# Performance work log

Hardware: AMD Instinct MI355X
Metric: run time of the kernel (lower is better)

## Reference

```python
import jax, jax.numpy as jnp
import numpy as np

EMB = 1024
HEAD = 64

def setup_inputs() -> dict:
    key = jax.random.key(0)
    ks = jax.random.split(key, 7)
    s = 1.0 / np.sqrt(EMB)
    X = jax.random.normal(ks[0], (4, 4096, EMB), dtype=jnp.float32)
    Wk = jax.random.uniform(ks[1], (EMB, HEAD), jnp.float32, -s, s)
    bk = jax.random.uniform(ks[2], (HEAD,), jnp.float32, -s, s)
    Wq = jax.random.uniform(ks[3], (EMB, HEAD), jnp.float32, -s, s)
    bq = jax.random.uniform(ks[4], (HEAD,), jnp.float32, -s, s)
    Wv = jax.random.uniform(ks[5], (EMB, HEAD), jnp.float32, -s, s)
    bv = jax.random.uniform(ks[6], (HEAD,), jnp.float32, -s, s)
    return {"X": X, "Wk": Wk, "bk": bk, "Wq": Wq, "bq": bq, "Wv": Wv, "bv": bv}

def reference(X, Wk, bk, Wq, bq, Wv, bv):
    # X: [B, S, E]; projections -> [B, S, H]
    k = X @ Wk + bk
    q = X @ Wq + bq
    v = X @ Wv + bv
    S = X.shape[1]
    scale = 1.0 / np.sqrt(HEAD).astype(np.float32)
    scores = jnp.einsum('bqh,bkh->bqk', q, k) * scale  # [B, S, S]
    causal = jnp.tril(jnp.ones((S, S), dtype=bool))
    scores = jnp.where(causal, scores, -jnp.inf)
    probs = jax.nn.softmax(scores, axis=-1)
    return jnp.einsum('bqk,bkh->bqh', probs, v)
```

## Files before the change

### kernel.cpp

```cpp
#include <hip/hip_runtime.h>

#define S_LEN 4096
#define EMBD  1024
#define HEADD 64

typedef __bf16 bf16x8 __attribute__((ext_vector_type(8)));
typedef float  f32x4  __attribute__((ext_vector_type(4)));

__device__ __forceinline__ unsigned short f2bf(float f) {
  union { float f; unsigned u; } x; x.f = f;
  unsigned r = x.u + 0x7FFFu + ((x.u >> 16) & 1u);
  return (unsigned short)(r >> 16);
}

__device__ __forceinline__ bf16x8 cvt8(f32x4 a, f32x4 b) {
  union { bf16x8 v; unsigned short s[8]; } u;
#pragma unroll
  for (int j = 0; j < 4; j++) { u.s[j] = f2bf(a[j]); u.s[4 + j] = f2bf(b[j]); }
  return u.v;
}

__device__ __forceinline__ unsigned fbits(float f) {
  union { float f; unsigned u; } x; x.f = f; return x.u;
}

__global__ void prep_w(const float* __restrict__ Wk, const float* __restrict__ bk,
                       const float* __restrict__ Wq, const float* __restrict__ bq,
                       const float* __restrict__ Wv, const float* __restrict__ bv,
                       unsigned short* __restrict__ wt, float* __restrict__ bias) {
  int n = blockIdx.x;
  int t = threadIdx.x;
  const float QSCALE = 0.125f * 1.44269504088896340736f;
  const float* W; const float* bsrc; int col; float s = 1.0f;
  if (n < 64)       { W = Wk; bsrc = bk; col = n; }
  else if (n < 128) { W = Wq; bsrc = bq; col = n - 64; s = QSCALE; }
  else              { W = Wv; bsrc = bv; col = n - 128; }
  for (int k = t; k < EMBD; k += 256)
    wt[n * EMBD + k] = f2bf(W[k * HEADD + col] * s);
  if (t == 0) bias[n] = bsrc[col] * s;
}

__global__ __launch_bounds__(256, 1) void proj_qkv(
    const float* __restrict__ X, const unsigned short* __restrict__ wt,
    const float* __restrict__ bias,
    unsigned short* __restrict__ qws, unsigned short* __restrict__ kws,
    unsigned short* __restrict__ vtws) {
  __shared__ unsigned short xs[64 * 512];

  const int tid = threadIdx.x;
  const int w = tid >> 6;
  const int lane = tid & 63;
  const int l15 = lane & 15, lg = lane >> 4;
  const int row0 = blockIdx.x * 64;

  const int sr = tid >> 5;
  const int sc = (tid & 31) * 8;

  const unsigned short* wp = wt + (size_t)(w * 48 + l15) * EMBD + lg * 8;

  f32x4 acc[4][3];
#pragma unroll
  for (int g = 0; g < 4; g++)
#pragma unroll
    for (int j = 0; j < 3; j++) acc[g][j] = (f32x4){0.f, 0.f, 0.f, 0.f};

  f32x4 la[16], lb[16];
#pragma unroll
  for (int it = 0; it < 16; it++) {
    const int r = (it & 7) * 8 + sr;
    const int c = (it >> 3) * 256 + sc;
    const float* src = X + (size_t)(row0 + r) * EMBD + c;
    la[it] = *(const f32x4*)src;
    lb[it] = *(const f32x4*)(src + 4);
  }
#pragma unroll
  for (int it = 0; it < 16; it++) {
    const int r = (it & 7) * 8 + sr;
    const int c = (it >> 3) * 256 + sc;
    int soff = (r << 9) + c;
    soff ^= (r & 7) << 3;
    *(bf16x8*)&xs[soff] = cvt8(la[it], lb[it]);
  }
  __syncthreads();

#pragma unroll
  for (int kc = 0; kc < 2; kc++) {
    if (kc + 1 < 2) {
#pragma unroll
      for (int it = 0; it < 16; it++) {
        const int r = (it & 7) * 8 + sr;
        const int c = 512 + (it >> 3) * 256 + sc;
        const float* src = X + (size_t)(row0 + r) * EMBD + c;
        la[it] = *(const f32x4*)src;
        lb[it] = *(const f32x4*)(src + 4);
      }
    }
    bf16x8 wf[2][3];
#pragma unroll
    for (int j = 0; j < 3; j++)
      wf[0][j] = *(const bf16x8*)(wp + (size_t)j * 16 * EMBD + kc * 512);
#pragma unroll
    for (int ss = 0; ss < 16; ss++) {
      const int cur = ss & 1;
      if (ss + 1 < 16) {
#pragma unroll
        for (int j = 0; j < 3; j++)
          wf[cur ^ 1][j] = *(const bf16x8*)(wp + (size_t)j * 16 * EMBD + kc * 512 + (ss + 1) * 32);
      }
      const int c = ss * 32 + lg * 8;
      bf16x8 a[4];
#pragma unroll
      for (int g = 0; g < 4; g++) {
        int so = ((g * 16 + l15) << 9) + c;
        so ^= (l15 & 7) << 3;
        a[g] = *(const bf16x8*)&xs[so];
      }
#pragma unroll
      for (int j = 0; j < 3; j++)
#pragma unroll
        for (int g = 0; g < 4; g++)
          acc[g][j] = __builtin_amdgcn_mfma_f32_16x16x32_bf16(a[g], wf[cur][j], acc[g][j], 0, 0, 0);
    }
    __syncthreads();
    if (kc + 1 < 2) {
#pragma unroll
      for (int it = 0; it < 16; it++) {
        const int r = (it & 7) * 8 + sr;
        const int c = (it >> 3) * 256 + sc;
        int soff = (r << 9) + c;
        soff ^= (r & 7) << 3;
        *(bf16x8*)&xs[soff] = cvt8(la[it], lb[it]);
      }
      __syncthreads();
    }
  }

#pragma unroll
  for (int g = 0; g < 4; g++) {
    const int crow0 = row0 + g * 16 + lg * 4;
#pragma unroll
    for (int j = 0; j < 3; j++) {
      const int nf = w * 3 + j;
      const int n = nf * 16 + l15;
      const float bs = bias[n];
      if (nf < 8) {
        unsigned short* dst = (nf < 4) ? kws : qws;
        const int nn = n & 63;
#pragma unroll
        for (int i = 0; i < 4; i++)
          dst[(size_t)(crow0 + i) * HEADD + nn] = f2bf(acc[g][j][i] + bs);
      } else {
        const int d = n - 128;
        const int bb = crow0 >> 12, sr2 = crow0 & 4095;
        union { unsigned long long pk; unsigned short s[4]; } u;
#pragma unroll
        for (int i = 0; i < 4; i++) u.s[i] = f2bf(acc[g][j][i] + bs);
        *(unsigned long long*)&vtws[((size_t)bb * HEADD + d) * S_LEN + sr2] = u.pk;
      }
    }
  }
}

__global__ __launch_bounds__(512, 1) void attn(
    const unsigned short* __restrict__ qws,
    const unsigned short* __restrict__ kws,
    const unsigned short* __restrict__ vtws,
    unsigned short* __restrict__ pO,
    float* __restrict__ pmv, float* __restrict__ plv) {
  __shared__ uint4 kvb[2][1024];
  __shared__ unsigned short pbl[8][16][72];

  const int tid = threadIdx.x;
  const int w = tid >> 6;
  const int lane = tid & 63;
  const int l15 = lane & 15, lg = lane >> 4;
  const int srow = tid >> 3;
  const int scol = (tid & 7) * 8;
  const int soff = ((srow * 128 + (tid & 7) * 16)) ^ ((srow & 7) << 4);

  const int id = blockIdx.x;
  const int b = id & 3;
  const int x = (id >> 2) & 15;
  const int h = id >> 6;

  const unsigned short* kb = kws + (size_t)b * S_LEN * HEADD;
  const unsigned short* vb = vtws + (size_t)b * HEADD * S_LEN;
  const unsigned short* qp = qws + (size_t)b * S_LEN * HEADD;

  const int PH = 31 - x, PL = x;
  const int tlPH = 2 * PH + 1;
  const int tlwH = 2 * PH + (w >> 2);
  const int tlwL = 2 * PL + (w >> 2);
  const int qbH = PH * 128 + w * 16;
  const int qbL = PL * 128 + w * 16;

  const unsigned short* qH = qp + (size_t)(qbH + l15) * HEADD + lg * 8;
  const unsigned short* qL = qp + (size_t)(qbL + l15) * HEADD + lg * 8;
  const bf16x8 bqH0 = *(const bf16x8*)qH, bqH1 = *(const bf16x8*)(qH + 32);
  const bf16x8 bqL0 = *(const bf16x8*)qL, bqL1 = *(const bf16x8*)(qL + 32);

  f32x4 oH[4], oL[4];
#pragma unroll
  for (int nd = 0; nd < 4; nd++) {
    oH[nd] = (f32x4){0.f, 0.f, 0.f, 0.f};
    oL[nd] = (f32x4){0.f, 0.f, 0.f, 0.f};
  }
  float mH = -3.0e38f, lH = 0.f, mL = -3.0e38f, lL = 0.f;

#define PROC(BQ0, BQ1, O, M, LL, QB, TLX, tt, base)                             \
  do {                                                                          \
    bf16x8 k0[4], k1[4], v0[4], v1[4];                                          \
    _Pragma("unroll")                                                           \
    for (int nf = 0; nf < 4; nf++) {                                            \
      const int r = nf * 16 + l15;                                              \
      const int sw = (l15 & 7) << 4;                                            \
      const int b0 = (r * 128 + lg * 16) ^ sw;                                  \
      const int b1 = (r * 128 + 64 + lg * 16) ^ sw;                             \
      k0[nf] = *(const bf16x8*)&base[b0];                                       \
      k1[nf] = *(const bf16x8*)&base[b1];                                       \
      v0[nf] = *(const bf16x8*)&base[8192 + b0];                                \
      v1[nf] = *(const bf16x8*)&base[8192 + b1];                                \
    }                                                                           \
    f32x4 sc[4];                                                                \
    __builtin_amdgcn_s_setprio(1);                                              \
    _Pragma("unroll")                                                           \
    for (int nf = 0; nf < 4; nf++) {                                            \
      f32x4 z = (f32x4){0.f, 0.f, 0.f, 0.f};                                    \
      z = __builtin_amdgcn_mfma_f32_16x16x32_bf16(k0[nf], BQ0, z, 0, 0, 0);     \
      sc[nf] = __builtin_amdgcn_mfma_f32_16x16x32_bf16(k1[nf], BQ1, z, 0, 0, 0);\
    }                                                                           \
    __builtin_amdgcn_s_setprio(0);                                              \
    if ((tt) == (TLX)) {                                                        \
      const int qa = (QB) + l15;                                                \
      _Pragma("unroll")                                                         \
      for (int nf = 0; nf < 4; nf++)                                            \
        _Pragma("unroll")                                                       \
        for (int i = 0; i < 4; i++)                                             \
          if ((tt) * 64 + nf * 16 + lg * 4 + i > qa) sc[nf][i] = -1.0e30f;      \
    }                                                                           \
    float pm = sc[0][0];                                                        \
    _Pragma("unroll")                                                           \
    for (int nf = 0; nf < 4; nf++)                                              \
      _Pragma("unroll")                                                         \
      for (int i = 0; i < 4; i++) pm = fmaxf(pm, sc[nf][i]);                    \
    if (!__all(pm <= M + 8.0f)) {                                               \
      float mx = fmaxf(pm, __shfl_xor(pm, 16));                                 \
      mx = fmaxf(mx, __shfl_xor(mx, 32));                                       \
      const float mn = fmaxf(M, mx);                                            \
      const float al = __builtin_amdgcn_exp2f(M - mn);                          \
      M = mn;                                                                   \
      LL *= al;                                                                 \
      float alr[4];                                                             \
      _Pragma("unroll")                                                         \
      for (int i = 0; i < 4; i++) alr[i] = __shfl(al, lg * 4 + i);              \
      _Pragma("unroll")                                                         \
      for (int nd = 0; nd < 4; nd++)                                            \
        _Pragma("unroll")                                                       \
        for (int i = 0; i < 4; i++) O[nd][i] *= alr[i];                         \
    }                                                                           \
    _Pragma("unroll")                                                           \
    for (int nf = 0; nf < 4; nf++) {                                            \
      f32x4 p;                                                                  \
      _Pragma("unroll")                                                         \
      for (int i = 0; i < 4; i++) p[i] = __builtin_amdgcn_exp2f(sc[nf][i] - M); \
      LL += p[0] + p[1] + p[2] + p[3];                                          \
      unsigned lo_ = __builtin_amdgcn_perm(fbits(p[1]) + 0x8000u,               \
                                           fbits(p[0]) + 0x8000u, 0x07060302u); \
      unsigned hi_ = __builtin_amdgcn_perm(fbits(p[3]) + 0x8000u,               \
                                           fbits(p[2]) + 0x8000u, 0x07060302u); \
      uint2 pk_; pk_.x = lo_; pk_.y = hi_;                                      \
      *(uint2*)&pbl[w][l15][nf * 16 + lg * 4] = pk_;                            \
    }                                                                           \
    const bf16x8 ap0 = *(const bf16x8*)&pbl[w][l15][lg * 8];                    \
    const bf16x8 ap1 = *(const bf16x8*)&pbl[w][l15][32 + lg * 8];               \
    __builtin_amdgcn_s_setprio(1);                                              \
    _Pragma("unroll")                                                           \
    for (int nd = 0; nd < 4; nd++) {                                            \
      f32x4 oo = __builtin_amdgcn_mfma_f32_16x16x32_bf16(ap0, v0[nd], O[nd], 0, 0, 0); \
      O[nd] = __builtin_amdgcn_mfma_f32_16x16x32_bf16(ap1, v1[nd], oo, 0, 0, 0);\
    }                                                                           \
    __builtin_amdgcn_s_setprio(0);                                              \
  } while (0)

#define LOADG(tt)                                                               \
  do {                                                                          \
    kreg = *(const uint4*)(kb + ((size_t)(tt) * 64 + srow) * HEADD + scol);     \
    vreg = *(const uint4*)(vb + (size_t)srow * S_LEN + (tt) * 64 + scol);       \
  } while (0)

#define WRITEL(bf)                                                              \
  do {                                                                          \
    unsigned char* d_ = (unsigned char*)kvb[bf];                                \
    *(uint4*)&d_[soff] = kreg;                                                  \
    *(uint4*)&d_[8192 + soff] = vreg;                                           \
  } while (0)

  {
    uint4 kreg, vreg;
    int t = h;
    LOADG(t);
    WRITEL(0);
    __syncthreads();
    int cur = 0;
#pragma unroll 1
    while (true) {
      const int tn = t + 4;
      const bool hn = tn <= tlPH;
      if (hn) LOADG(tn);
      {
        const unsigned char* base = (const unsigned char*)kvb[cur];
        if (t <= tlwH) PROC(bqH0, bqH1, oH, mH, lH, qbH, tlwH, t, base);
        if (t <= tlwL) PROC(bqL0, bqL1, oL, mL, lL, qbL, tlwL, t, base);
      }
      if (!hn) break;
      WRITEL(cur ^ 1);
      __syncthreads();
      cur ^= 1;
      t = tn;
    }
  }

  lH += __shfl_xor(lH, 16);
  lH += __shfl_xor(lH, 32);
  lL += __shfl_xor(lL, 16);
  lL += __shfl_xor(lL, 32);
  const size_t pbH = (size_t)(h * 4 + b) * S_LEN + qbH;
  const size_t pbL = (size_t)(h * 4 + b) * S_LEN + qbL;
  if (lane < 16) {
    pmv[pbH + lane] = mH; plv[pbH + lane] = lH;
    pmv[pbL + lane] = mL; plv[pbL + lane] = lL;
  }
#pragma unroll
  for (int nd = 0; nd < 4; nd++)
#pragma unroll
    for (int i = 0; i < 4; i++) {
      pO[(pbH + lg * 4 + i) * 64 + nd * 16 + l15] = f2bf(oH[nd][i]);
      pO[(pbL + lg * 4 + i) * 64 + nd * 16 + l15] = f2bf(oL[nd][i]);
    }
#undef PROC
#undef LOADG
#undef WRITEL
}

__global__ __launch_bounds__(256) void merge_attn(
    const unsigned short* __restrict__ pO,
    const float* __restrict__ pmv, const float* __restrict__ plv,
    float* __restrict__ out) {
  const int row = blockIdx.x * 64 + (threadIdx.x >> 2);
  const int q = threadIdx.x & 3;
  float mh[4], lh[4];
  float M = -3.0e38f;
#pragma unroll
  for (int hh = 0; hh < 4; hh++) {
    mh[hh] = pmv[hh * 16384 + row];
    lh[hh] = plv[hh * 16384 + row];
    M = fmaxf(M, mh[hh]);
  }
  float Lt = 0.f, a[4];
#pragma unroll
  for (int hh = 0; hh < 4; hh++) {
    a[hh] = __builtin_amdgcn_exp2f(mh[hh] - M);
    Lt += a[hh] * lh[hh];
  }
  const float iL = 1.0f / Lt;
  float acc[16];
#pragma unroll
  for (int c = 0; c < 16; c++) acc[c] = 0.f;
#pragma unroll
  for (int hh = 0; hh < 4; hh++) {
    const unsigned short* src = pO + ((size_t)hh * 16384 + row) * 64 + q * 16;
    const uint4 u0 = *(const uint4*)(src);
    const uint4 u1 = *(const uint4*)(src + 8);
    const unsigned* uu0 = (const unsigned*)&u0;
    const unsigned* uu1 = (const unsigned*)&u1;
#pragma unroll
    for (int j = 0; j < 4; j++) {
      union { unsigned u; float f; } e0, e1, e2, e3;
      e0.u = uu0[j] << 16;  e1.u = uu0[j] & 0xffff0000u;
      e2.u = uu1[j] << 16;  e3.u = uu1[j] & 0xffff0000u;
      acc[j * 2 + 0] += e0.f * a[hh];
      acc[j * 2 + 1] += e1.f * a[hh];
      acc[8 + j * 2 + 0] += e2.f * a[hh];
      acc[8 + j * 2 + 1] += e3.f * a[hh];
    }
  }
  float* dst = out + (size_t)row * 64 + q * 16;
#pragma unroll
  for (int c = 0; c < 16; c++) dst[c] = acc[c] * iL;
}

extern "C" void kernel_launch(void* const* d_in, const int* in_sizes, int n_in,
                              void* d_out, int out_size, void* d_ws, size_t ws_size,
                              hipStream_t stream) {
  const float* X  = (const float*)d_in[0];
  const float* Wk = (const float*)d_in[1];
  const float* bk = (const float*)d_in[2];
  const float* Wq = (const float*)d_in[3];
  const float* bq = (const float*)d_in[4];
  const float* Wv = (const float*)d_in[5];
  const float* bv = (const float*)d_in[6];
  float* out = (float*)d_out;

  char* ws = (char*)d_ws;
  unsigned short* kws  = (unsigned short*)(ws);
  unsigned short* qws  = (unsigned short*)(ws + (2u << 20));
  unsigned short* vtws = (unsigned short*)(ws + (4u << 20));
  unsigned short* wt   = (unsigned short*)(ws + (6u << 20));
  float*          bias = (float*)(ws + (6u << 20) + (512u << 10));
  unsigned short* pO   = (unsigned short*)(ws + (8u << 20));
  float*          pmv  = (float*)(ws + (16u << 20));
  float*          plv  = (float*)(ws + (17u << 20));

  prep_w<<<dim3(192), dim3(256), 0, stream>>>(Wk, bk, Wq, bq, Wv, bv, wt, bias);
  proj_qkv<<<dim3(256), dim3(256), 0, stream>>>(X, wt, bias, qws, kws, vtws);
  attn<<<dim3(256), dim3(512), 0, stream>>>(qws, kws, vtws, pO, pmv, plv);
  merge_attn<<<dim3(256), dim3(256), 0, stream>>>(pO, pmv, plv, out);
}
```

Measured before the change: 61.11 us.

## Split attention work into 64-row query tiles with one tile per warp

The attention kernel now launches 512 blocks instead of 256. Each warp handles a single 16-row query slice, taken from either the high or the low 64-row tile of a paired causal range, rather than processing both a high and a low slice. This halves per-warp register state (one accumulator set), and launch bounds now allow two blocks per CU to raise occupancy. The cost is that each block's shared K/V tile is reused by fewer query rows, and warps in the low half sit idle once their causal range ends.

```diff
diff --git a/kernel.cpp b/kernel.cpp
--- a/kernel.cpp
+++ b/kernel.cpp
@@ -161,7 +161,7 @@
   }
 }
 
-__global__ __launch_bounds__(512, 1) void attn(
+__global__ __launch_bounds__(512, 2) void attn(
     const unsigned short* __restrict__ qws,
     const unsigned short* __restrict__ kws,
     const unsigned short* __restrict__ vtws,
@@ -180,34 +180,29 @@
 
   const int id = blockIdx.x;
   const int b = id & 3;
-  const int x = (id >> 2) & 15;
-  const int h = id >> 6;
+  const int x = (id >> 2) & 31;
+  const int h = id >> 7;
 
   const unsigned short* kb = kws + (size_t)b * S_LEN * HEADD;
   const unsigned short* vb = vtws + (size_t)b * HEADD * S_LEN;
   const unsigned short* qp = qws + (size_t)b * S_LEN * HEADD;
 
-  const int PH = 31 - x, PL = x;
-  const int tlPH = 2 * PH + 1;
-  const int tlwH = 2 * PH + (w >> 2);
-  const int tlwL = 2 * PL + (w >> 2);
-  const int qbH = PH * 128 + w * 16;
-  const int qbL = PL * 128 + w * 16;
-
-  const unsigned short* qH = qp + (size_t)(qbH + l15) * HEADD + lg * 8;
-  const unsigned short* qL = qp + (size_t)(qbL + l15) * HEADD + lg * 8;
-  const bf16x8 bqH0 = *(const bf16x8*)qH, bqH1 = *(const bf16x8*)(qH + 32);
-  const bf16x8 bqL0 = *(const bf16x8*)qL, bqL1 = *(const bf16x8*)(qL + 32);
-
-  f32x4 oH[4], oL[4];
-#pragma unroll
-  for (int nd = 0; nd < 4; nd++) {
-    oH[nd] = (f32x4){0.f, 0.f, 0.f, 0.f};
-    oL[nd] = (f32x4){0.f, 0.f, 0.f, 0.f};
-  }
-  float mH = -3.0e38f, lH = 0.f, mL = -3.0e38f, lL = 0.f;
-
-#define PROC(BQ0, BQ1, O, M, LL, QB, TLX, tt, base)                             \
+  const int isL = w >> 2;
+  const int P = isL ? x : 63 - x;
+  const int qb = P * 64 + (w & 3) * 16;
+  const int myTL = P;
+  const int tlPH = 63 - x;
+
+  const unsigned short* qptr = qp + (size_t)(qb + l15) * HEADD + lg * 8;
+  const bf16x8 bq0 = *(const bf16x8*)qptr;
+  const bf16x8 bq1 = *(const bf16x8*)(qptr + 32);
+
+  f32x4 o[4];
+#pragma unroll
+  for (int nd = 0; nd < 4; nd++) o[nd] = (f32x4){0.f, 0.f, 0.f, 0.f};
+  float m = -3.0e38f, l = 0.f;
+
+#define PROC(tt, base)                                                          \
   do {                                                                          \
     bf16x8 k0[4], k1[4], v0[4], v1[4];                                          \
     _Pragma("unroll")                                                           \
@@ -226,12 +221,12 @@
     _Pragma("unroll")                                                           \
     for (int nf = 0; nf < 4; nf++) {                                            \
       f32x4 z = (f32x4){0.f, 0.f, 0.f, 0.f};                                    \
-      z = __builtin_amdgcn_mfma_f32_16x16x32_bf16(k0[nf], BQ0, z, 0, 0, 0);     \
-      sc[nf] = __builtin_amdgcn_mfma_f32_16x16x32_bf16(k1[nf], BQ1, z, 0, 0, 0);\
+      z = __builtin_amdgcn_mfma_f32_16x16x32_bf16(k0[nf], bq0, z, 0, 0, 0);     \
+      sc[nf] = __builtin_amdgcn_mfma_f32_16x16x32_bf16(k1[nf], bq1, z, 0, 0, 0);\
     }                                                                           \
     __builtin_amdgcn_s_setprio(0);                                              \
-    if ((tt) == (TLX)) {                                                        \
-      const int qa = (QB) + l15;                                                \
+    if ((tt) == myTL) {                                                         \
+      const int qa = qb + l15;                                                  \
       _Pragma("unroll")                                                         \
       for (int nf = 0; nf < 4; nf++)                                            \
         _Pragma("unroll")                                                       \
@@ -243,27 +238,27 @@
     for (int nf = 0; nf < 4; nf++)                                              \
       _Pragma("unroll")                                                         \
       for (int i = 0; i < 4; i++) pm = fmaxf(pm, sc[nf][i]);                    \
-    if (!__all(pm <= M + 8.0f)) {                                               \
+    if (!__all(pm <= m + 8.0f)) {                                               \
       float mx = fmaxf(pm, __shfl_xor(pm, 16));                                 \
       mx = fmaxf(mx, __shfl_xor(mx, 32));                                       \
-      const float mn = fmaxf(M, mx);                                            \
-      const float al = __builtin_amdgcn_exp2f(M - mn);                          \
-      M = mn;                                                                   \
-      LL *= al;                                                                 \
+      const float mn = fmaxf(m, mx);                                            \
+      const float al = __builtin_amdgcn_exp2f(m - mn);                          \
+      m = mn;                                                                   \
+      l *= al;                                                                  \
       float alr[4];                                                             \
       _Pragma("unroll")                                                         \
       for (int i = 0; i < 4; i++) alr[i] = __shfl(al, lg * 4 + i);              \
       _Pragma("unroll")                                                         \
       for (int nd = 0; nd < 4; nd++)                                            \
         _Pragma("unroll")                                                       \
-        for (int i = 0; i < 4; i++) O[nd][i] *= alr[i];                         \
+        for (int i = 0; i < 4; i++) o[nd][i] *= alr[i];                         \
     }                                                                           \
     _Pragma("unroll")                                                           \
     for (int nf = 0; nf < 4; nf++) {                                            \
       f32x4 p;                                                                  \
       _Pragma("unroll")                                                         \
-      for (int i = 0; i < 4; i++) p[i] = __builtin_amdgcn_exp2f(sc[nf][i] - M); \
-      LL += p[0] + p[1] + p[2] + p[3];                                          \
+      for (int i = 0; i < 4; i++) p[i] = __builtin_amdgcn_exp2f(sc[nf][i] - m); \
+      l += p[0] + p[1] + p[2] + p[3];                                           \
       unsigned lo_ = __builtin_amdgcn_perm(fbits(p[1]) + 0x8000u,               \
                                            fbits(p[0]) + 0x8000u, 0x07060302u); \
       unsigned hi_ = __builtin_amdgcn_perm(fbits(p[3]) + 0x8000u,               \
@@ -276,8 +271,8 @@
     __builtin_amdgcn_s_setprio(1);                                              \
     _Pragma("unroll")                                                           \
     for (int nd = 0; nd < 4; nd++) {                                            \
-      f32x4 oo = __builtin_amdgcn_mfma_f32_16x16x32_bf16(ap0, v0[nd], O[nd], 0, 0, 0); \
-      O[nd] = __builtin_amdgcn_mfma_f32_16x16x32_bf16(ap1, v1[nd], oo, 0, 0, 0);\
+      f32x4 oo = __builtin_amdgcn_mfma_f32_16x16x32_bf16(ap0, v0[nd], o[nd], 0, 0, 0); \
+      o[nd] = __builtin_amdgcn_mfma_f32_16x16x32_bf16(ap1, v1[nd], oo, 0, 0, 0);\
     }                                                                           \
     __builtin_amdgcn_s_setprio(0);                                              \
   } while (0)
@@ -309,8 +304,7 @@
       if (hn) LOADG(tn);
       {
         const unsigned char* base = (const unsigned char*)kvb[cur];
-        if (t <= tlwH) PROC(bqH0, bqH1, oH, mH, lH, qbH, tlwH, t, base);
-        if (t <= tlwL) PROC(bqL0, bqL1, oL, mL, lL, qbL, tlwL, t, base);
+        if (t <= myTL) PROC(t, base);
       }
       if (!hn) break;
       WRITEL(cur ^ 1);
@@ -320,23 +314,15 @@
     }
   }
 
-  lH += __shfl_xor(lH, 16);
-  lH += __shfl_xor(lH, 32);
-  lL += __shfl_xor(lL, 16);
-  lL += __shfl_xor(lL, 32);
-  const size_t pbH = (size_t)(h * 4 + b) * S_LEN + qbH;
-  const size_t pbL = (size_t)(h * 4 + b) * S_LEN + qbL;
-  if (lane < 16) {
-    pmv[pbH + lane] = mH; plv[pbH + lane] = lH;
-    pmv[pbL + lane] = mL; plv[pbL + lane] = lL;
-  }
+  l += __shfl_xor(l, 16);
+  l += __shfl_xor(l, 32);
+  const size_t pbase = (size_t)(h * 4 + b) * S_LEN + qb;
+  if (lane < 16) { pmv[pbase + lane] = m; plv[pbase + lane] = l; }
 #pragma unroll
   for (int nd = 0; nd < 4; nd++)
 #pragma unroll
-    for (int i = 0; i < 4; i++) {
-      pO[(pbH + lg * 4 + i) * 64 + nd * 16 + l15] = f2bf(oH[nd][i]);
-      pO[(pbL + lg * 4 + i) * 64 + nd * 16 + l15] = f2bf(oL[nd][i]);
-    }
+    for (int i = 0; i < 4; i++)
+      pO[(pbase + lg * 4 + i) * 64 + nd * 16 + l15] = f2bf(o[nd][i]);
 #undef PROC
 #undef LOADG
 #undef WRITEL
@@ -413,6 +399,6 @@
 
   prep_w<<<dim3(192), dim3(256), 0, stream>>>(Wk, bk, Wq, bq, Wv, bv, wt, bias);
   proj_qkv<<<dim3(256), dim3(256), 0, stream>>>(X, wt, bias, qws, kws, vtws);
-  attn<<<dim3(256), dim3(512), 0, stream>>>(qws, kws, vtws, pO, pmv, plv);
+  attn<<<dim3(512), dim3(512), 0, stream>>>(qws, kws, vtws, pO, pmv, plv);
   merge_attn<<<dim3(256), dim3(256), 0, stream>>>(pO, pmv, plv, out);
 }
```

After: 69.33 us. +13.5%, slower.
